# Optimization experiments

Measured on AMD Instinct MI355X. Metric: run time of the kernel, lower is better.

Reference implementation:

```python
import jax, jax.numpy as jnp
import numpy as np

MARGIN = 1.0
EPS = 1e-6  # torch F.pairwise_distance eps


def setup_inputs() -> dict:
    key = jax.random.key(0)
    k1, k2, k3, k4, k5 = jax.random.split(key, 5)
    B, C, H, W = 128, 1024, 14, 14
    return {
        "feat": jax.random.normal(k1, (B, C, H, W), dtype=jnp.float32),
        "feat_p": jax.random.normal(k2, (B, C, H, W), dtype=jnp.float32),
        "avg_feat": jax.random.normal(k3, (2, C, 1, 1), dtype=jnp.float32),
        "qual": jax.random.randint(k4, (B,), 0, 2, dtype=jnp.int64),
        "label": jax.random.randint(k5, (B,), 0, 2, dtype=jnp.int64),
    }


def reference(feat, feat_p, avg_feat, qual, label):
    # AdaptiveAvgPool2d(1): global average over H, W -> [B, C]
    f = feat.mean(axis=(2, 3))
    fp = feat_p.mean(axis=(2, 3))
    # torch code concatenates f[qual==1] and fp[qual==0]; since qual is binary
    # this is a permutation of per-sample selections and the final sum is
    # permutation-invariant, so select per-sample instead of gathering.
    sel = jnp.where((qual == 1)[:, None], f, fp)  # [B, C] anchors
    af = avg_feat[:, :, 0, 0]  # [2, C]
    pos = af[label]            # [B, C]
    neg = af[1 - label]        # [B, C]
    # TripletMarginLoss on [C,1,1] tensors: pairwise_distance reduces the last
    # dim (size 1) with p=2, i.e. d = |a - b + eps| elementwise; then mean
    # over the C*1 elements, summed over the batch.
    d_ap = jnp.abs(sel - pos + EPS)
    d_an = jnp.abs(sel - neg + EPS)
    per_sample = jnp.maximum(d_ap - d_an + MARGIN, 0.0).mean(axis=1)  # [B]
    return per_sample.sum()
```

## Files before the change

kernel.cpp:

```cpp
#include <hip/hip_runtime.h>


#define B_ 128
#define C_ 1024
#define HW_ 196
#define NF4_ 49
#define CPW_ 8
#define WPB_ 4
#define CPB_ (CPW_*WPB_)
#define BLKS_PER_B_ (C_/CPB_)
#define NBLOCKS_ (B_*BLKS_PER_B_)

__global__ __launch_bounds__(256) void loss_partial_kernel(
    const float* __restrict__ feat, const float* __restrict__ feat_p,
    const float* __restrict__ af, const int* __restrict__ qual,
    const int* __restrict__ label, float* __restrict__ ws)
{
    const int blk  = blockIdx.x;
    const int b    = blk >> 5;
    const int cg   = blk & 31;
    const int wave = threadIdx.x >> 6;
    const int lane = threadIdx.x & 63;
    const int c0   = cg * CPB_ + wave * CPW_;

    const int q   = qual[b];
    const int lab = label[b];
    const float* base = (q == 1 ? feat : feat_p) + (size_t)b * (C_ * HW_);
    const float* pos_row = af + (size_t)lab * C_;
    const float* neg_row = af + (size_t)(1 - lab) * C_;

    float hacc = 0.0f;
    #pragma unroll
    for (int j = 0; j < CPW_; ++j) {
        const int c = c0 + j;
        const float4* p = (const float4*)(base + (size_t)c * HW_);
        float4 v = make_float4(0.f, 0.f, 0.f, 0.f);
        if (lane < NF4_) v = p[lane];
        float s = (v.x + v.y) + (v.z + v.w);
        #pragma unroll
        for (int off = 32; off > 0; off >>= 1)
            s += __shfl_xor(s, off, 64);
        const float mean = s * (1.0f / 196.0f);
        const float pos = pos_row[c];
        const float neg = neg_row[c];
        const float dap = fabsf(mean - pos + 1e-6f);
        const float dan = fabsf(mean - neg + 1e-6f);
        hacc += fmaxf(dap - dan + 1.0f, 0.0f);
    }

    __shared__ float sred[WPB_];
    if (lane == 0) sred[wave] = hacc;
    __syncthreads();
    if (threadIdx.x == 0) {
        ws[blk] = (sred[0] + sred[1]) + (sred[2] + sred[3]);
    }
}

__global__ __launch_bounds__(256) void final_reduce_kernel(
    const float* __restrict__ ws, float* __restrict__ out)
{
    const int tid = threadIdx.x;
    float s = 0.0f;
    #pragma unroll
    for (int i = 0; i < NBLOCKS_ / 256; ++i)
        s += ws[tid + i * 256];
    #pragma unroll
    for (int off = 32; off > 0; off >>= 1)
        s += __shfl_xor(s, off, 64);
    __shared__ float sred[WPB_];
    if ((tid & 63) == 0) sred[tid >> 6] = s;
    __syncthreads();
    if (tid == 0)
        out[0] = ((sred[0] + sred[1]) + (sred[2] + sred[3])) * (1.0f / (float)C_);
}

extern "C" void kernel_launch(void* const* d_in, const int* in_sizes, int n_in,
                              void* d_out, int out_size, void* d_ws, size_t ws_size,
                              hipStream_t stream) {
    const float* feat   = (const float*)d_in[0];
    const float* feat_p = (const float*)d_in[1];
    const float* af     = (const float*)d_in[2];
    const int*   qual   = (const int*)d_in[3];
    const int*   label  = (const int*)d_in[4];
    float* out = (float*)d_out;
    float* ws  = (float*)d_ws;

    loss_partial_kernel<<<NBLOCKS_, 256, 0, stream>>>(feat, feat_p, af, qual, label, ws);
    final_reduce_kernel<<<1, 256, 0, stream>>>(ws, out);
}
```

Before: 199.8 us.

## Assign one channel per thread with sequential float4 loads instead of wave-per-channel

```diff
diff --git a/kernel.cpp b/kernel.cpp
--- a/kernel.cpp
+++ b/kernel.cpp
@@ -5,69 +5,57 @@
 #define C_ 1024
 #define HW_ 196
 #define NF4_ 49
-#define CPW_ 8
-#define WPB_ 4
-#define CPB_ (CPW_*WPB_)
-#define BLKS_PER_B_ (C_/CPB_)
-#define NBLOCKS_ (B_*BLKS_PER_B_)
+#define TPB_ 256
+#define NBLOCKS_ (B_ * C_ / TPB_)
 
-__global__ __launch_bounds__(256) void loss_partial_kernel(
+__global__ __launch_bounds__(TPB_) void loss_partial_kernel(
     const float* __restrict__ feat, const float* __restrict__ feat_p,
     const float* __restrict__ af, const int* __restrict__ qual,
     const int* __restrict__ label, float* __restrict__ ws)
 {
-    const int blk  = blockIdx.x;
-    const int b    = blk >> 5;
-    const int cg   = blk & 31;
-    const int wave = threadIdx.x >> 6;
-    const int lane = threadIdx.x & 63;
-    const int c0   = cg * CPB_ + wave * CPW_;
+    const int blk = blockIdx.x;
+    const int b   = blk >> 2;
+    const int c   = ((blk & 3) << 8) | threadIdx.x;
 
     const int q   = qual[b];
     const int lab = label[b];
-    const float* base = (q == 1 ? feat : feat_p) + (size_t)b * (C_ * HW_);
-    const float* pos_row = af + (size_t)lab * C_;
-    const float* neg_row = af + (size_t)(1 - lab) * C_;
+    const float* sel = (q == 1 ? feat : feat_p);
+    const float4* p = (const float4*)(sel + ((size_t)b * C_ + c) * HW_);
 
-    float hacc = 0.0f;
+    float s0 = 0.f, s1 = 0.f, s2 = 0.f, s3 = 0.f;
     #pragma unroll
-    for (int j = 0; j < CPW_; ++j) {
-        const int c = c0 + j;
-        const float4* p = (const float4*)(base + (size_t)c * HW_);
-        float4 v = make_float4(0.f, 0.f, 0.f, 0.f);
-        if (lane < NF4_) v = p[lane];
-        float s = (v.x + v.y) + (v.z + v.w);
-        #pragma unroll
-        for (int off = 32; off > 0; off >>= 1)
-            s += __shfl_xor(s, off, 64);
-        const float mean = s * (1.0f / 196.0f);
-        const float pos = pos_row[c];
-        const float neg = neg_row[c];
-        const float dap = fabsf(mean - pos + 1e-6f);
-        const float dan = fabsf(mean - neg + 1e-6f);
-        hacc += fmaxf(dap - dan + 1.0f, 0.0f);
+    for (int i = 0; i < NF4_; ++i) {
+        float4 v = p[i];
+        s0 += v.x; s1 += v.y; s2 += v.z; s3 += v.w;
     }
+    const float mean = ((s0 + s1) + (s2 + s3)) * (1.0f / 196.0f);
 
-    __shared__ float sred[WPB_];
-    if (lane == 0) sred[wave] = hacc;
+    const float pos = af[lab * C_ + c];
+    const float neg = af[(1 - lab) * C_ + c];
+    const float dap = fabsf(mean - pos + 1e-6f);
+    const float dan = fabsf(mean - neg + 1e-6f);
+    float h = fmaxf(dap - dan + 1.0f, 0.0f);
+
+    #pragma unroll
+    for (int off = 32; off > 0; off >>= 1)
+        h += __shfl_xor(h, off, 64);
+    __shared__ float sred[TPB_ / 64];
+    const int wave = threadIdx.x >> 6;
+    if ((threadIdx.x & 63) == 0) sred[wave] = h;
     __syncthreads();
-    if (threadIdx.x == 0) {
+    if (threadIdx.x == 0)
         ws[blk] = (sred[0] + sred[1]) + (sred[2] + sred[3]);
-    }
 }
 
-__global__ __launch_bounds__(256) void final_reduce_kernel(
+__global__ __launch_bounds__(TPB_) void final_reduce_kernel(
     const float* __restrict__ ws, float* __restrict__ out)
 {
     const int tid = threadIdx.x;
-    float s = 0.0f;
-    #pragma unroll
-    for (int i = 0; i < NBLOCKS_ / 256; ++i)
-        s += ws[tid + i * 256];
+    float s = ws[tid] + ws[tid + TPB_];
     #pragma unroll
     for (int off = 32; off > 0; off >>= 1)
         s += __shfl_xor(s, off, 64);
-    __shared__ float sred[WPB_];
+    __shared__ float sred[TPB_ / 64];
     if ((tid & 63) == 0) sred[tid >> 6] = s;
     __syncthreads();
     if (tid == 0)
@@ -85,6 +73,6 @@
     float* out = (float*)d_out;
     float* ws  = (float*)d_ws;
 
-    loss_partial_kernel<<<NBLOCKS_, 256, 0, stream>>>(feat, feat_p, af, qual, label, ws);
-    final_reduce_kernel<<<1, 256, 0, stream>>>(ws, out);
+    loss_partial_kernel<<<NBLOCKS_, TPB_, 0, stream>>>(feat, feat_p, af, qual, label, ws);
+    final_reduce_kernel<<<1, TPB_, 0, stream>>>(ws, out);
 }
```

Result: slower. 218.7 us (+9.5%).
